# Kernel optimization log

Hardware: AMD Instinct MI355X
Metric: run time of the kernel (lower is better)

Reference implementation:

```python
import jax, jax.numpy as jnp
import numpy as np

N2, S2, M2 = 20000, 16000, 4000   # hop-2 frontier, hop-2 src fanout, hop-2 dst nodes
S1, M1 = 3500, 1024               # hop-1 src fanout, final batch
D_IN, D_H = 128, 128              # input_dim, internal_dim


def setup_inputs() -> dict:
    key = jax.random.key(0)
    ks = jax.random.split(key, 9)
    return {
        "src_nodes": jax.random.normal(ks[0], (N2, D_IN), dtype=jnp.float32),
        "dstsrc2src_1": jax.random.randint(ks[1], (S1,), 0, M2, dtype=jnp.int64),
        "dstsrc2src_2": jax.random.randint(ks[2], (S2,), 0, N2, dtype=jnp.int64),
        "dstsrc2dst_1": jax.random.randint(ks[3], (M1,), 0, M2, dtype=jnp.int64),
        "dstsrc2dst_2": jax.random.randint(ks[4], (M2,), 0, N2, dtype=jnp.int64),
        "dif_mat_1": jax.random.uniform(ks[5], (M1, S1), dtype=jnp.float32),
        "dif_mat_2": jax.random.uniform(ks[6], (M2, S2), dtype=jnp.float32),
        "w1": jax.random.normal(ks[7], (2 * D_IN, D_H), dtype=jnp.float32) * 0.06,
        "w2": jax.random.normal(ks[8], (2 * D_H, D_H), dtype=jnp.float32) * 0.06,
    }


def _mean_aggregate(feats, dstsrc2src, dstsrc2dst, dif_mat, w):
    # gather -> diffusion matmul -> concat -> linear -> relu
    dst_features = feats[dstsrc2dst]               # [M, d]
    src_features = feats[dstsrc2src]               # [S, d]
    aggregated = dif_mat @ src_features            # [M, d]
    concatenated = jnp.concatenate([aggregated, dst_features], axis=1)  # [M, 2d]
    return jax.nn.relu(concatenated @ w)           # [M, d_out]


def reference(src_nodes, dstsrc2src_1, dstsrc2src_2, dstsrc2dst_1,
              dstsrc2dst_2, dif_mat_1, dif_mat_2, w1, w2):
    # GraphSage.call: hop-2 aggregator first (with *_2 inputs), then hop-1.
    x = _mean_aggregate(src_nodes, dstsrc2src_2, dstsrc2dst_2, dif_mat_2, w1)
    x = _mean_aggregate(x, dstsrc2src_1, dstsrc2dst_1, dif_mat_1, w2)
    return x
```

## Files before the change

kernel.cpp:

```cpp
#include <hip/hip_runtime.h>

typedef __bf16 bf16x8 __attribute__((ext_vector_type(8)));
typedef float  f32x4  __attribute__((ext_vector_type(4)));
typedef unsigned short u16;
typedef u16 u16x8 __attribute__((ext_vector_type(8)));

__device__ __forceinline__ u16 f2bf(float f) {
    unsigned u = __builtin_bit_cast(unsigned, f);
    return (u16)((u + 0x7FFFu + ((u >> 16) & 1u)) >> 16);
}

__device__ __forceinline__ bf16x8 packA(f32x4 a0, f32x4 a1) {
    u16x8 h;
    h[0]=f2bf(a0[0]); h[1]=f2bf(a0[1]); h[2]=f2bf(a0[2]); h[3]=f2bf(a0[3]);
    h[4]=f2bf(a1[0]); h[5]=f2bf(a1[1]); h[6]=f2bf(a1[2]); h[7]=f2bf(a1[3]);
    return __builtin_bit_cast(bf16x8, h);
}

__global__ __launch_bounds__(256) void gather_bt(
    const float* __restrict__ feats, const int* __restrict__ idx,
    u16* __restrict__ Bt, int Kcnt, int Kpad)
{
    __shared__ u16 st[128][66];
    const int tid = threadIdx.x;
    const int k0  = blockIdx.x * 64;

#pragma unroll
    for (int r2 = 0; r2 < 64; r2 += 2) {
        int r = r2 + (tid >> 7);
        int c = tid & 127;
        int k = k0 + r;
        float v = 0.f;
        if (k < Kcnt) v = feats[(size_t)idx[k] * 128 + c];
        st[c][r] = f2bf(v);
    }
    __syncthreads();

#pragma unroll
    for (int p = 0; p < 4; ++p) {
        int n  = p * 32 + (tid >> 3);
        int kk = (tid & 7) * 8;
        u16x8 v;
#pragma unroll
        for (int j = 0; j < 8; ++j) v[j] = st[n][kk + j];
        *(u16x8*)(Bt + (size_t)n * Kpad + k0 + kk) = v;
    }
}

__global__ __launch_bounds__(256, 2) void gemm_bt(
    const float* __restrict__ A, const u16* __restrict__ Bt,
    float* __restrict__ C, int M, int K, int Kpad, int mspan)
{
    const int wid  = threadIdx.x >> 6;
    const int lane = threadIdx.x & 63;
    const int l15  = lane & 15;
    const int lhi  = lane >> 4;

    const int row0 = blockIdx.x * 64 + wid * 16;
    const int macro_total = (K + 255) >> 8;
    int m0 = blockIdx.y * mspan;
    int m1 = m0 + mspan; if (m1 > macro_total) m1 = macro_total;
    if (m0 >= m1) return;

    f32x4 acc[8];
#pragma unroll
    for (int j = 0; j < 8; ++j) acc[j] = (f32x4){0.f, 0.f, 0.f, 0.f};

    const int rA = min(row0 + l15, M - 1);
    const float* __restrict__ ap  = A + (size_t)rA * K;
    const u16*   __restrict__ btl = Bt + (size_t)l15 * Kpad + lhi * 8;

    bf16x8 bcur[8];
    {
        const int kf = m0 << 8;
#pragma unroll
        for (int cf = 0; cf < 8; ++cf)
            bcur[cf] = __builtin_bit_cast(bf16x8,
                *(const u16x8*)(btl + (size_t)cf * 16 * Kpad + kf));
    }

    for (int m = m0; m < m1; ++m) {
        const int kbase = m << 8;

        f32x4 araw[16];
        if (kbase + 256 <= K) {
#pragma unroll
            for (int j = 0; j < 8; ++j) {
                const int koff = kbase + j * 32 + lhi * 8;
                araw[2 * j]     = *(const f32x4*)(ap + koff);
                araw[2 * j + 1] = *(const f32x4*)(ap + koff + 4);
            }
        } else {
#pragma unroll
            for (int j = 0; j < 8; ++j) {
                const int koff = kbase + j * 32 + lhi * 8;
                f32x4 a0, a1;
#pragma unroll
                for (int e = 0; e < 4; ++e) {
                    a0[e] = (koff + e     < K) ? ap[koff + e]     : 0.f;
                    a1[e] = (koff + 4 + e < K) ? ap[koff + 4 + e] : 0.f;
                }
                araw[2 * j] = a0; araw[2 * j + 1] = a1;
            }
        }

#pragma unroll
        for (int j = 0; j < 8; ++j) {
            const int knext = kbase + j * 32 + 32;
            bf16x8 bnxt[8];
#pragma unroll
            for (int cf = 0; cf < 8; ++cf)
                bnxt[cf] = __builtin_bit_cast(bf16x8,
                    *(const u16x8*)(btl + (size_t)cf * 16 * Kpad + knext));

            const bf16x8 af = packA(araw[2 * j], araw[2 * j + 1]);
#pragma unroll
            for (int cf = 0; cf < 8; ++cf)
                acc[cf] = __builtin_amdgcn_mfma_f32_16x16x32_bf16(af, bcur[cf], acc[cf], 0, 0, 0);

#pragma unroll
            for (int cf = 0; cf < 8; ++cf) bcur[cf] = bnxt[cf];
        }
    }

#pragma unroll
    for (int cf = 0; cf < 8; ++cf)
#pragma unroll
        for (int i = 0; i < 4; ++i) {
            int r = row0 + lhi * 4 + i;
            if (r < M)
                atomicAdd(C + (size_t)r * 128 + cf * 16 + l15, acc[cf][i]);
        }
}

__global__ __launch_bounds__(256) void dense_relu(
    const float* __restrict__ agg, const float* __restrict__ fsrc,
    const int* __restrict__ didx, const float* __restrict__ w,
    float* __restrict__ out, int M)
{
    __shared__ float sb[32][257];
    const int tid  = threadIdx.x;
    const int row0 = blockIdx.x * 32;

    for (int i = tid; i < 32 * 32; i += 256) {
        int r = i >> 5, c4 = (i & 31) << 2;
        int gr = row0 + r;
        f32x4 v = (f32x4){0.f, 0.f, 0.f, 0.f};
        if (gr < M) v = *(const f32x4*)(agg + (size_t)gr * 128 + c4);
        sb[r][c4 + 0] = v[0]; sb[r][c4 + 1] = v[1];
        sb[r][c4 + 2] = v[2]; sb[r][c4 + 3] = v[3];
    }
    for (int i = tid; i < 32 * 32; i += 256) {
        int r = i >> 5, c4 = (i & 31) << 2;
        int gr = row0 + r;
        int sr = (gr < M) ? didx[gr] : 0;
        f32x4 v = *(const f32x4*)(fsrc + (size_t)sr * 128 + c4);
        sb[r][128 + c4 + 0] = v[0]; sb[r][128 + c4 + 1] = v[1];
        sb[r][128 + c4 + 2] = v[2]; sb[r][128 + c4 + 3] = v[3];
    }
    __syncthreads();

    const int colg = (tid & 15) << 3;
    const int r0l  = (tid >> 4) * 2;
    float acc0[8], acc1[8];
#pragma unroll
    for (int c = 0; c < 8; ++c) { acc0[c] = 0.f; acc1[c] = 0.f; }

#pragma unroll 4
    for (int j = 0; j < 256; ++j) {
        f32x4 wa = *(const f32x4*)(w + j * 128 + colg);
        f32x4 wb = *(const f32x4*)(w + j * 128 + colg + 4);
        float a0 = sb[r0l][j];
        float a1 = sb[r0l + 1][j];
#pragma unroll
        for (int c = 0; c < 4; ++c) {
            acc0[c]     += a0 * wa[c];  acc0[c + 4] += a0 * wb[c];
            acc1[c]     += a1 * wa[c];  acc1[c + 4] += a1 * wb[c];
        }
    }

    int gr0 = row0 + r0l;
    if (gr0 < M) {
#pragma unroll
        for (int c = 0; c < 8; ++c)
            out[(size_t)gr0 * 128 + colg + c] = fmaxf(acc0[c], 0.f);
    }
    int gr1 = gr0 + 1;
    if (gr1 < M) {
#pragma unroll
        for (int c = 0; c < 8; ++c)
            out[(size_t)gr1 * 128 + colg + c] = fmaxf(acc1[c], 0.f);
    }
}

extern "C" void kernel_launch(void* const* d_in, const int* in_sizes, int n_in,
                              void* d_out, int out_size, void* d_ws, size_t ws_size,
                              hipStream_t stream)
{
    const float* src_nodes = (const float*)d_in[0];
    const int*   s1idx     = (const int*)d_in[1];
    const int*   s2idx     = (const int*)d_in[2];
    const int*   d1idx     = (const int*)d_in[3];
    const int*   d2idx     = (const int*)d_in[4];
    const float* dif1      = (const float*)d_in[5];
    const float* dif2      = (const float*)d_in[6];
    const float* w1        = (const float*)d_in[7];
    const float* w2        = (const float*)d_in[8];
    float*       out       = (float*)d_out;

    const int S2 = 16000, M2 = 4000, S1 = 3500, M1 = 1024;
    const int K2 = 16000, K1 = 3500;
    const int Kpad2 = 16128;
    const int Kpad1 = 3584;

    char* ws = (char*)d_ws;
    size_t off = 0;
    float* agg2 = (float*)(ws + off); off += (size_t)M2 * 128 * 4;
    float* agg1 = (float*)(ws + off); off += (size_t)M1 * 128 * 4;
    float* x    = (float*)(ws + off); off += (size_t)M2 * 128 * 4;
    u16*   Bt2  = (u16*)(ws + off);   off += (size_t)128 * Kpad2 * 2 + 512;
    u16*   Bt1  = (u16*)(ws + off);   off += (size_t)128 * Kpad1 * 2 + 512;

    hipMemsetAsync(agg2, 0, (size_t)(M2 + M1) * 128 * 4, stream);

    gather_bt<<<Kpad2 / 64, 256, 0, stream>>>(src_nodes, s2idx, Bt2, S2, Kpad2);

    {
        dim3 grid((M2 + 63) / 64, 8);
        gemm_bt<<<grid, 256, 0, stream>>>(dif2, Bt2, agg2, M2, K2, Kpad2, 8);
    }

    dense_relu<<<(M2 + 31) / 32, 256, 0, stream>>>(agg2, src_nodes, d2idx, w1, x, M2);

    gather_bt<<<Kpad1 / 64, 256, 0, stream>>>(x, s1idx, Bt1, S1, Kpad1);

    {
        dim3 grid((M1 + 63) / 64, 14);
        gemm_bt<<<grid, 256, 0, stream>>>(dif1, Bt1, agg1, M1, K1, Kpad1, 1);
    }

    dense_relu<<<(M1 + 31) / 32, 256, 0, stream>>>(agg1, x, d1idx, w2, out, M1);
}
```

Baseline: 588.1 us.

## Stage A tiles via async global-to-LDS loads and pre-pack B in fragment order

The GEMM now streams the fp32 diffusion-matrix tiles into double-buffered, XOR-swizzled shared memory using global_load_lds, replacing per-lane direct global reads. The gather kernel writes B in an MFMA-fragment-packed layout so each lane reads contiguous 16-byte chunks, removing the strided Kpad rows. It also switches to native bf16 conversion. The aim is to improve coalescing and overlap A loads with MFMA work. The cost is 64 KB of LDS per block, which may reduce occupancy, plus extra barriers per macro-step.

```diff
diff --git a/kernel.cpp b/kernel.cpp
--- a/kernel.cpp
+++ b/kernel.cpp
@@ -5,23 +5,18 @@
 typedef unsigned short u16;
 typedef u16 u16x8 __attribute__((ext_vector_type(8)));
 
-__device__ __forceinline__ u16 f2bf(float f) {
-    unsigned u = __builtin_bit_cast(unsigned, f);
-    return (u16)((u + 0x7FFFu + ((u >> 16) & 1u)) >> 16);
-}
-
 __device__ __forceinline__ bf16x8 packA(f32x4 a0, f32x4 a1) {
-    u16x8 h;
-    h[0]=f2bf(a0[0]); h[1]=f2bf(a0[1]); h[2]=f2bf(a0[2]); h[3]=f2bf(a0[3]);
-    h[4]=f2bf(a1[0]); h[5]=f2bf(a1[1]); h[6]=f2bf(a1[2]); h[7]=f2bf(a1[3]);
-    return __builtin_bit_cast(bf16x8, h);
+    bf16x8 r;
+    r[0] = (__bf16)a0[0]; r[1] = (__bf16)a0[1]; r[2] = (__bf16)a0[2]; r[3] = (__bf16)a0[3];
+    r[4] = (__bf16)a1[0]; r[5] = (__bf16)a1[1]; r[6] = (__bf16)a1[2]; r[7] = (__bf16)a1[3];
+    return r;
 }
 
 __global__ __launch_bounds__(256) void gather_bt(
     const float* __restrict__ feats, const int* __restrict__ idx,
-    u16* __restrict__ Bt, int Kcnt, int Kpad)
-{
-    __shared__ u16 st[128][66];
+    u16* __restrict__ BP, int Kcnt)
+{
+    __shared__ u16 st[128][72];
     const int tid = threadIdx.x;
     const int k0  = blockIdx.x * 64;
 
@@ -32,88 +27,110 @@
         int k = k0 + r;
         float v = 0.f;
         if (k < Kcnt) v = feats[(size_t)idx[k] * 128 + c];
-        st[c][r] = f2bf(v);
+        st[c][r] = __builtin_bit_cast(u16, (__bf16)v);
     }
     __syncthreads();
 
-#pragma unroll
-    for (int p = 0; p < 4; ++p) {
-        int n  = p * 32 + (tid >> 3);
-        int kk = (tid & 7) * 8;
-        u16x8 v;
-#pragma unroll
-        for (int j = 0; j < 8; ++j) v[j] = st[n][kk + j];
-        *(u16x8*)(Bt + (size_t)n * Kpad + k0 + kk) = v;
+    const int s_local = tid >> 7;
+    const int cf      = (tid >> 4) & 7;
+    const int l15     = tid & 15;
+    const int s       = blockIdx.x * 2 + s_local;
+    const int n       = cf * 16 + l15;
+#pragma unroll
+    for (int lhi = 0; lhi < 4; ++lhi) {
+        u16x8 v = *(const u16x8*)&st[n][s_local * 32 + lhi * 8];
+        *(u16x8*)(BP + ((size_t)(s * 8 + cf) * 64 + lhi * 16 + l15) * 8) = v;
     }
 }
 
 __global__ __launch_bounds__(256, 2) void gemm_bt(
-    const float* __restrict__ A, const u16* __restrict__ Bt,
-    float* __restrict__ C, int M, int K, int Kpad, int mspan)
-{
-    const int wid  = threadIdx.x >> 6;
-    const int lane = threadIdx.x & 63;
+    const float* __restrict__ A, const u16* __restrict__ BP,
+    float* __restrict__ C, int M, int K, int nmacro, int mspan, int nktot)
+{
+    __shared__ float As[2][64][128];
+    const int tid  = threadIdx.x;
+    const int wid  = tid >> 6;
+    const int lane = tid & 63;
     const int l15  = lane & 15;
     const int lhi  = lane >> 4;
-
+    const int swz  = l15 & 7;
     const int row0 = blockIdx.x * 64 + wid * 16;
-    const int macro_total = (K + 255) >> 8;
+
     int m0 = blockIdx.y * mspan;
-    int m1 = m0 + mspan; if (m1 > macro_total) m1 = macro_total;
+    int m1 = m0 + mspan; if (m1 > nmacro) m1 = nmacro;
     if (m0 >= m1) return;
 
+    auto stage = [&](int m, int buf) {
+        const int kbase = m << 7;
+        if (kbase + 128 <= K) {
+#pragma unroll
+            for (int i = 0; i < 8; ++i) {
+                const int lr = wid * 16 + i * 2 + (lane >> 5);
+                const int ar = min(blockIdx.x * 64 + lr, M - 1);
+                const float* src = A + (size_t)ar * K + kbase
+                                 + (((lane & 31) ^ (lr & 7)) << 2);
+                __builtin_amdgcn_global_load_lds(
+                    (const __attribute__((address_space(1))) void*)src,
+                    (__attribute__((address_space(3))) void*)&As[buf][wid * 16 + i * 2][0],
+                    16, 0, 0);
+            }
+        } else {
+#pragma unroll
+            for (int i = 0; i < 8; ++i) {
+                const int lr = wid * 16 + i * 2 + (lane >> 5);
+                const int ar = min(blockIdx.x * 64 + lr, M - 1);
+                const int u  = lane & 31;
+                const float* src = A + (size_t)ar * K + kbase + (u << 2);
+                f32x4 v;
+#pragma unroll
+                for (int e = 0; e < 4; ++e) {
+                    int kk = kbase + (u << 2) + e;
+                    v[e] = (kk < K) ? src[e] : 0.f;
+                }
+                *(f32x4*)&As[buf][lr][(u ^ (lr & 7)) << 2] = v;
+            }
+        }
+    };
+
+    stage(m0, 0);
+
     f32x4 acc[8];
 #pragma unroll
     for (int j = 0; j < 8; ++j) acc[j] = (f32x4){0.f, 0.f, 0.f, 0.f};
 
-    const int rA = min(row0 + l15, M - 1);
-    const float* __restrict__ ap  = A + (size_t)rA * K;
-    const u16*   __restrict__ btl = Bt + (size_t)l15 * Kpad + lhi * 8;
+    const u16* __restrict__ bp_lane = BP + (size_t)lane * 8;
 
     bf16x8 bcur[8];
     {
-        const int kf = m0 << 8;
+        const int s_first = m0 << 2;
 #pragma unroll
         for (int cf = 0; cf < 8; ++cf)
             bcur[cf] = __builtin_bit_cast(bf16x8,
-                *(const u16x8*)(btl + (size_t)cf * 16 * Kpad + kf));
-    }
+                *(const u16x8*)(bp_lane + ((size_t)(s_first * 8 + cf) << 9)));
+    }
+
+    __builtin_amdgcn_s_waitcnt(0x0F70);
+    __syncthreads();
 
     for (int m = m0; m < m1; ++m) {
-        const int kbase = m << 8;
-
-        f32x4 araw[16];
-        if (kbase + 256 <= K) {
-#pragma unroll
-            for (int j = 0; j < 8; ++j) {
-                const int koff = kbase + j * 32 + lhi * 8;
-                araw[2 * j]     = *(const f32x4*)(ap + koff);
-                araw[2 * j + 1] = *(const f32x4*)(ap + koff + 4);
-            }
-        } else {
-#pragma unroll
-            for (int j = 0; j < 8; ++j) {
-                const int koff = kbase + j * 32 + lhi * 8;
-                f32x4 a0, a1;
-#pragma unroll
-                for (int e = 0; e < 4; ++e) {
-                    a0[e] = (koff + e     < K) ? ap[koff + e]     : 0.f;
-                    a1[e] = (koff + 4 + e < K) ? ap[koff + 4 + e] : 0.f;
-                }
-                araw[2 * j] = a0; araw[2 * j + 1] = a1;
-            }
-        }
-
-#pragma unroll
-        for (int j = 0; j < 8; ++j) {
-            const int knext = kbase + j * 32 + 32;
+        const int buf = (m - m0) & 1;
+        if (m + 1 < m1) stage(m + 1, buf ^ 1);
+
+#pragma unroll
+        for (int j = 0; j < 4; ++j) {
+            const int s  = (m << 2) + j;
+            int sn = s + 1; if (sn > nktot - 1) sn = nktot - 1;
             bf16x8 bnxt[8];
 #pragma unroll
             for (int cf = 0; cf < 8; ++cf)
                 bnxt[cf] = __builtin_bit_cast(bf16x8,
-                    *(const u16x8*)(btl + (size_t)cf * 16 * Kpad + knext));
-
-            const bf16x8 af = packA(araw[2 * j], araw[2 * j + 1]);
+                    *(const u16x8*)(bp_lane + ((size_t)(sn * 8 + cf) << 9)));
+
+            const int ub = (j << 3) + (lhi << 1);
+            const f32x4 a0 = *(const f32x4*)&As[buf][wid * 16 + l15][(ub ^ swz) << 2];
+            const f32x4 a1 = *(const f32x4*)&As[buf][wid * 16 + l15][((ub + 1) ^ swz) << 2];
+            const bf16x8 af = packA(a0, a1);
+
 #pragma unroll
             for (int cf = 0; cf < 8; ++cf)
                 acc[cf] = __builtin_amdgcn_mfma_f32_16x16x32_bf16(af, bcur[cf], acc[cf], 0, 0, 0);
@@ -121,13 +138,16 @@
 #pragma unroll
             for (int cf = 0; cf < 8; ++cf) bcur[cf] = bnxt[cf];
         }
+
+        __builtin_amdgcn_s_waitcnt(0x0F70);
+        __syncthreads();
     }
 
 #pragma unroll
     for (int cf = 0; cf < 8; ++cf)
 #pragma unroll
         for (int i = 0; i < 4; ++i) {
-            int r = row0 + lhi * 4 + i;
+            const int r = row0 + lhi * 4 + i;
             if (r < M)
                 atomicAdd(C + (size_t)r * 128 + cf * 16 + l15, acc[cf][i]);
         }
@@ -208,36 +228,31 @@
     const float* w2        = (const float*)d_in[8];
     float*       out       = (float*)d_out;
 
-    const int S2 = 16000, M2 = 4000, S1 = 3500, M1 = 1024;
+    const int M2 = 4000, M1 = 1024;
     const int K2 = 16000, K1 = 3500;
-    const int Kpad2 = 16128;
-    const int Kpad1 = 3584;
+    const int NK2 = 500, NK1 = 112;
 
     char* ws = (char*)d_ws;
     size_t off = 0;
     float* agg2 = (float*)(ws + off); off += (size_t)M2 * 128 * 4;
     float* agg1 = (float*)(ws + off); off += (size_t)M1 * 128 * 4;
     float* x    = (float*)(ws + off); off += (size_t)M2 * 128 * 4;
-    u16*   Bt2  = (u16*)(ws + off);   off += (size_t)128 * Kpad2 * 2 + 512;
-    u16*   Bt1  = (u16*)(ws + off);   off += (size_t)128 * Kpad1 * 2 + 512;
+    u16*   BP2  = (u16*)(ws + off);   off += (size_t)NK2 * 8 * 64 * 8 * 2;
+    u16*   BP1  = (u16*)(ws + off);   off += (size_t)NK1 * 8 * 64 * 8 * 2;
 
     hipMemsetAsync(agg2, 0, (size_t)(M2 + M1) * 128 * 4, stream);
 
-    gather_bt<<<Kpad2 / 64, 256, 0, stream>>>(src_nodes, s2idx, Bt2, S2, Kpad2);
-
+    gather_bt<<<NK2 / 2, 256, 0, stream>>>(src_nodes, s2idx, BP2, K2);
     {
         dim3 grid((M2 + 63) / 64, 8);
-        gemm_bt<<<grid, 256, 0, stream>>>(dif2, Bt2, agg2, M2, K2, Kpad2, 8);
-    }
-
+        gemm_bt<<<grid, 256, 0, stream>>>(dif2, BP2, agg2, M2, K2, 125, 16, NK2);
+    }
     dense_relu<<<(M2 + 31) / 32, 256, 0, stream>>>(agg2, src_nodes, d2idx, w1, x, M2);
 
-    gather_bt<<<Kpad1 / 64, 256, 0, stream>>>(x, s1idx, Bt1, S1, Kpad1);
-
+    gather_bt<<<NK1 / 2, 256, 0, stream>>>(x, s1idx, BP1, K1);
     {
         dim3 grid((M1 + 63) / 64, 14);
-        gemm_bt<<<grid, 256, 0, stream>>>(dif1, Bt1, agg1, M1, K1, Kpad1, 1);
-    }
-
+        gemm_bt<<<grid, 256, 0, stream>>>(dif1, BP1, agg1, M1, K1, 28, 2, NK1);
+    }
     dense_relu<<<(M1 + 31) / 32, 256, 0, stream>>>(agg1, x, d1idx, w2, out, M1);
 }
```

New measurement: 522.0 us. 1.13x faster.
